# Kernel tuning notes

Measured on AMD Instinct MI355X. Metric: run time of the kernel, lower is better.

Reference implementation:

```python
import jax, jax.numpy as jnp
import numpy as np

B, T, C = 4, 2048, 1024
N_HEAD = 16
HEAD_DIM = C // N_HEAD
SCALE = 1.0 / np.sqrt(HEAD_DIM).astype(np.float32)


def setup_inputs() -> dict:
    key = jax.random.key(0)
    k1, k2, k3 = jax.random.split(key, 3)
    x = jax.random.normal(k1, (B, T, C), dtype=jnp.float32)
    # torch Linear weights: [out_features, in_features], scaled init
    w_qkv = jax.random.normal(k2, (3 * C, C), dtype=jnp.float32) * (1.0 / np.sqrt(C))
    w_out = jax.random.normal(k3, (C, C), dtype=jnp.float32) * (1.0 / np.sqrt(C))
    b_out = jnp.zeros((C,), dtype=jnp.float32)
    return {"x": x, "w_qkv": w_qkv, "w_out": w_out, "b_out": b_out}


def reference(x, w_qkv, w_out, b_out):
    Bsz, Tlen, Cdim = x.shape
    qkv = jnp.einsum('btc,oc->bto', x, w_qkv)  # [B,T,3C]
    q, k, v = jnp.split(qkv, 3, axis=-1)
    # [B,H,T,D]
    def heads(t):
        return t.reshape(Bsz, Tlen, N_HEAD, HEAD_DIM).transpose(0, 2, 1, 3)
    q, k, v = heads(q), heads(k), heads(v)
    att = jnp.einsum('bhqd,bhkd->bhqk', q, k) * SCALE  # [B,H,T,T]
    causal = jnp.tril(jnp.ones((Tlen, Tlen), dtype=bool))
    att = jnp.where(causal[None, None], att, -jnp.inf)
    att = jax.nn.softmax(att, axis=-1)
    out = jnp.einsum('bhqk,bhkd->bhqd', att, v)
    out = out.transpose(0, 2, 1, 3).reshape(Bsz, Tlen, Cdim)
    out = jnp.einsum('btc,oc->bto', out, w_out) + b_out
    return out
```

## Files before the change

### kernel.cpp

```cpp
#include <hip/hip_runtime.h>
#include <stdint.h>


typedef __attribute__((ext_vector_type(8))) short bf16x8;
typedef __attribute__((ext_vector_type(4))) float f32x4;

#define EXP2F(x) __builtin_amdgcn_exp2f(x)
#define SL2E 0.18033688011112042f
#define FIXED_M 15.0f

template <bool B> struct BoolC { static constexpr bool value = B; };

__device__ __forceinline__ short f2bf(float f) {
  union { float f; unsigned u; } c; c.f = f;
  unsigned u = c.u;
  unsigned r = (u + 0x7fffu + ((u >> 16) & 1u)) >> 16;
  return (short)(unsigned short)r;
}

__device__ __forceinline__ void softmax_pack(const f32x4* sc, bf16x8& pa0, bf16x8& pa1) {
  union U { int i[4]; bf16x8 v; };
  U u0, u1;
#pragma unroll
  for (int j = 0; j < 4; ++j) {
    float p0 = EXP2F(sc[j][0]);
    float p1 = EXP2F(sc[j][1]);
    float p2 = EXP2F(sc[j][2]);
    float p3 = EXP2F(sc[j][3]);
    int w0, w1;
    asm("v_cvt_pk_bf16_f32 %0, %1, %2" : "=v"(w0) : "v"(p0), "v"(p1));
    asm("v_cvt_pk_bf16_f32 %0, %1, %2" : "=v"(w1) : "v"(p2), "v"(p3));
    if (j < 2) { u0.i[j * 2] = w0; u0.i[j * 2 + 1] = w1; }
    else       { u1.i[(j - 2) * 2] = w0; u1.i[(j - 2) * 2 + 1] = w1; }
  }
  pa0 = u0.v;
  pa1 = u1.v;
}

__device__ __forceinline__ void llds16(const short* g, short* l) {
  __builtin_amdgcn_global_load_lds(
      (const __attribute__((address_space(1))) unsigned int*)g,
      (__attribute__((address_space(3))) unsigned int*)l, 16, 0, 0);
}

__global__ __launch_bounds__(256) void cast_f32_to_bf16(
    const float* __restrict__ src, short* __restrict__ dst, int n4) {
  int i = blockIdx.x * 256 + threadIdx.x;
  if (i >= n4) return;
  float4 f = ((const float4*)src)[i];
  short4 o;
  o.x = f2bf(f.x); o.y = f2bf(f.y); o.z = f2bf(f.z); o.w = f2bf(f.w);
  ((short4*)dst)[i] = o;
}

__global__ __launch_bounds__(256) void gemm_qkv(
    const short* __restrict__ A, const short* __restrict__ Bw,
    short* __restrict__ Qo, short* __restrict__ Ko, short* __restrict__ Vt) {
  const int K = 1024;
  __shared__ short smem[17408];
  const int tid = threadIdx.x;
  const int lane = tid & 63;
  const int wave = tid >> 6;
  const int m0 = blockIdx.y * 128;
  const int n0 = blockIdx.x * 128;
  const int wm = (wave >> 1) * 64;
  const int wn = (wave & 1) * 64;
  const int mrow = lane & 15;
  const int kq = lane >> 4;

  f32x4 acc[4][4];
#pragma unroll
  for (int i = 0; i < 4; ++i)
#pragma unroll
    for (int j = 0; j < 4; ++j) acc[i][j] = (f32x4){0.f, 0.f, 0.f, 0.f};

  auto stage = [&](int it, int buf) {
#pragma unroll
    for (int call = 0; call < 2; ++call) {
      const int cb = call * 256 + wave * 64;
      const int c = cb + lane;
      const int row = c >> 2;
      const int scol = (c & 3) ^ (row & 3);
      llds16(A + (size_t)(m0 + row) * K + it * 32 + scol * 8,
             &smem[buf * 8192 + cb * 8]);
      llds16(Bw + (size_t)(n0 + row) * K + it * 32 + scol * 8,
             &smem[buf * 8192 + 4096 + cb * 8]);
    }
  };

  stage(0, 0);
  __syncthreads();

  for (int it = 0; it < 32; ++it) {
    const int buf = it & 1;
    if (it < 31) stage(it + 1, buf ^ 1);
    const short* lA = &smem[buf * 8192];
    const short* lB = &smem[buf * 8192 + 4096];
    bf16x8 af[4], bfr[4];
#pragma unroll
    for (int i = 0; i < 4; ++i) {
      const int row = wm + i * 16 + mrow;
      af[i] = *(const bf16x8*)&lA[row * 32 + ((kq ^ (row & 3)) * 8)];
    }
#pragma unroll
    for (int j = 0; j < 4; ++j) {
      const int row = wn + j * 16 + mrow;
      bfr[j] = *(const bf16x8*)&lB[row * 32 + ((kq ^ (row & 3)) * 8)];
    }
#pragma unroll
    for (int i = 0; i < 4; ++i)
#pragma unroll
      for (int j = 0; j < 4; ++j)
        acc[i][j] = __builtin_amdgcn_mfma_f32_16x16x32_bf16(af[i], bfr[j], acc[i][j], 0, 0, 0);
    __syncthreads();
  }

  const int b = m0 >> 11;
  if (n0 < 2048) {
    short* lC = smem;
#pragma unroll
    for (int i = 0; i < 4; ++i) {
      const int row = wm + i * 16 + kq * 4;
#pragma unroll
      for (int j = 0; j < 4; ++j) {
        const int col = wn + j * 16 + mrow;
        const float sc_ = (((n0 + col) >> 10) == 1) ? SL2E : 1.0f;
#pragma unroll
        for (int r = 0; r < 4; ++r)
          lC[(row + r) * 132 + col] = f2bf(acc[i][j][r] * sc_);
      }
    }
    __syncthreads();
#pragma unroll
    for (int call = 0; call < 8; ++call) {
      const int cc = call * 256 + tid;
      const int row = cc >> 4;
      const int t = (m0 + row) & 2047;
      const int o = n0 + (cc & 15) * 8;
      const int c = o & 1023;
      const int h = c >> 6;
      const int d = c & 63;
      short* dst = (o >> 10) == 0 ? Qo : Ko;
      bf16x8 val = *(const bf16x8*)&lC[row * 132 + (cc & 15) * 8];
      *(bf16x8*)(dst + ((size_t)(b * 16 + h) * 2048 + t) * 64 + d) = val;
    }
  } else {
    short* lCt = smem;
#pragma unroll
    for (int i = 0; i < 4; ++i) {
      const int row = wm + i * 16 + kq * 4;
#pragma unroll
      for (int j = 0; j < 4; ++j) {
        const int col = wn + j * 16 + mrow;
#pragma unroll
        for (int r = 0; r < 4; ++r)
          lCt[col * 136 + row + r] = f2bf(acc[i][j][r]);
      }
    }
    __syncthreads();
#pragma unroll
    for (int call = 0; call < 8; ++call) {
      const int cc = call * 256 + tid;
      const int col = cc >> 4;
      const int tg = cc & 15;
      const int o = n0 + col;
      const int d = o & 63;
      const int h = (o >> 6) & 15;
      const int t = (m0 & 2047) + tg * 8;
      bf16x8 val = *(const bf16x8*)&lCt[col * 136 + tg * 8];
      *(bf16x8*)(Vt + ((size_t)(b * 16 + h) * 64 + d) * 2048 + t) = val;
    }
  }
}

__global__ __launch_bounds__(256) void gemm_out(
    const short* __restrict__ A, const short* __restrict__ Bw,
    const float* __restrict__ bias, float* __restrict__ Out) {
  const int K = 1024;
  __shared__ short smem[16384];
  const int tid = threadIdx.x;
  const int lane = tid & 63;
  const int wave = tid >> 6;
  const int m0 = blockIdx.y * 128;
  const int n0 = blockIdx.x * 128;
  const int wm = (wave >> 1) * 64;
  const int wn = (wave & 1) * 64;
  const int mrow = lane & 15;
  const int kq = lane >> 4;

  f32x4 acc[4][4];
#pragma unroll
  for (int i = 0; i < 4; ++i)
#pragma unroll
    for (int j = 0; j < 4; ++j) acc[i][j] = (f32x4){0.f, 0.f, 0.f, 0.f};

  auto stage = [&](int it, int buf) {
#pragma unroll
    for (int call = 0; call < 2; ++call) {
      const int cb = call * 256 + wave * 64;
      const int c = cb + lane;
      const int row = c >> 2;
      const int scol = (c & 3) ^ (row & 3);
      llds16(A + (size_t)(m0 + row) * K + it * 32 + scol * 8,
             &smem[buf * 8192 + cb * 8]);
      llds16(Bw + (size_t)(n0 + row) * K + it * 32 + scol * 8,
             &smem[buf * 8192 + 4096 + cb * 8]);
    }
  };

  stage(0, 0);
  __syncthreads();

  for (int it = 0; it < 32; ++it) {
    const int buf = it & 1;
    if (it < 31) stage(it + 1, buf ^ 1);
    const short* lA = &smem[buf * 8192];
    const short* lB = &smem[buf * 8192 + 4096];
    bf16x8 af[4], bfr[4];
#pragma unroll
    for (int i = 0; i < 4; ++i) {
      const int row = wm + i * 16 + mrow;
      af[i] = *(const bf16x8*)&lA[row * 32 + ((kq ^ (row & 3)) * 8)];
    }
#pragma unroll
    for (int j = 0; j < 4; ++j) {
      const int row = wn + j * 16 + mrow;
      bfr[j] = *(const bf16x8*)&lB[row * 32 + ((kq ^ (row & 3)) * 8)];
    }
#pragma unroll
    for (int i = 0; i < 4; ++i)
#pragma unroll
      for (int j = 0; j < 4; ++j)
        acc[i][j] = __builtin_amdgcn_mfma_f32_16x16x32_bf16(af[i], bfr[j], acc[i][j], 0, 0, 0);
    __syncthreads();
  }

#pragma unroll
  for (int i = 0; i < 4; ++i) {
    const int m = m0 + wm + i * 16 + kq * 4;
#pragma unroll
    for (int j = 0; j < 4; ++j) {
      const int n = n0 + wn + j * 16 + mrow;
      const float bb = bias[n];
#pragma unroll
      for (int r = 0; r < 4; ++r)
        Out[(size_t)(m + r) * 1024 + n] = acc[i][j][r] + bb;
    }
  }
}

__global__ __launch_bounds__(256) void flash_attn(
    const short* __restrict__ Qg, const short* __restrict__ Kg,
    const short* __restrict__ Vtg, short* __restrict__ Og) {
  const int T = 2048;
  __shared__ short lK[2][64 * 64];
  __shared__ short lVt[2][64 * 64];
  const int tid = threadIdx.x;
  const int lane = tid & 63;
  const int wave = tid >> 6;
  const int bh = blockIdx.x;
  const int bx = blockIdx.y;
  const int mrow = lane & 15;
  const int kq = lane >> 4;
  const int swz = mrow & 7;
  const size_t base = (size_t)bh * T * 64;
  const size_t vbase = (size_t)bh * 64 * T;

  const int qt0 = bx;
  const int qt1 = 31 - bx;

  const bf16x8 ones = {0x3F80, 0x3F80, 0x3F80, 0x3F80, 0x3F80, 0x3F80, 0x3F80, 0x3F80};

  bf16x8 aq0_0, aq1_0, aq0_1, aq1_1;
  {
    const short* qp0 = Qg + base + (size_t)(qt0 * 64 + wave * 16 + mrow) * 64 + kq * 8;
    aq0_0 = *(const bf16x8*)qp0;
    aq1_0 = *(const bf16x8*)(qp0 + 32);
    const short* qp1 = Qg + base + (size_t)(qt1 * 64 + wave * 16 + mrow) * 64 + kq * 8;
    aq0_1 = *(const bf16x8*)qp1;
    aq1_1 = *(const bf16x8*)(qp1 + 32);
  }

  f32x4 acc0[4], acc1[4], lac0, lac1;
  lac0 = (f32x4){0.f, 0.f, 0.f, 0.f};
  lac1 = (f32x4){0.f, 0.f, 0.f, 0.f};
#pragma unroll
  for (int jd = 0; jd < 4; ++jd) {
    acc0[jd] = (f32x4){0.f, 0.f, 0.f, 0.f};
    acc1[jd] = (f32x4){0.f, 0.f, 0.f, 0.f};
  }

  auto stage = [&](int nt, int buf) {
#pragma unroll
    for (int call = 0; call < 2; ++call) {
      const int cb = call * 256 + wave * 64;
      const int c = cb + lane;
      const int row = c >> 3;
      const int scol = (c & 7) ^ (row & 7);
      const int grow = (row & 0x23) | ((row & 0x0C) << 1) | ((row & 0x10) >> 2);
      llds16(Kg + base + (size_t)(nt * 64 + grow) * 64 + scol * 8, &lK[buf][cb * 8]);
      llds16(Vtg + vbase + (size_t)row * T + nt * 64 + scol * 8, &lVt[buf][cb * 8]);
    }
  };

  stage(0, 0);
  __syncthreads();

  auto seg = [&](auto A, const short* K_, const short* Vt_, int kt) {
    constexpr bool ACT0 = decltype(A)::value;
    f32x4 sc0[4], sc1[4];
#pragma unroll
    for (int j = 0; j < 4; ++j) {
      const short* krow = &K_[(j * 16 + mrow) * 64];
      bf16x8 kb0 = *(const bf16x8*)&krow[(kq ^ swz) * 8];
      bf16x8 kb1 = *(const bf16x8*)&krow[((4 + kq) ^ swz) * 8];
      __builtin_amdgcn_s_setprio(1);
      f32x4 ss = (f32x4){-FIXED_M, -FIXED_M, -FIXED_M, -FIXED_M};
      ss = __builtin_amdgcn_mfma_f32_16x16x32_bf16(kb0, aq0_1, ss, 0, 0, 0);
      ss = __builtin_amdgcn_mfma_f32_16x16x32_bf16(kb1, aq1_1, ss, 0, 0, 0);
      sc1[j] = ss;
      if constexpr (ACT0) {
        f32x4 s2 = (f32x4){-FIXED_M, -FIXED_M, -FIXED_M, -FIXED_M};
        s2 = __builtin_amdgcn_mfma_f32_16x16x32_bf16(kb0, aq0_0, s2, 0, 0, 0);
        s2 = __builtin_amdgcn_mfma_f32_16x16x32_bf16(kb1, aq1_0, s2, 0, 0, 0);
        sc0[j] = s2;
      }
      __builtin_amdgcn_s_setprio(0);
    }

    if (kt == qt1) {
      const int qcol = qt1 * 64 + wave * 16 + mrow;
#pragma unroll
      for (int j = 0; j < 4; ++j) {
        const int keyb = kt * 64 + ((j & 2) << 4) + (kq << 3) + ((j & 1) << 2);
#pragma unroll
        for (int r = 0; r < 4; ++r)
          if (keyb + r > qcol) sc1[j][r] = -1e30f;
      }
    }
    if constexpr (ACT0) {
      if (kt == qt0) {
        const int qcol = qt0 * 64 + wave * 16 + mrow;
#pragma unroll
        for (int j = 0; j < 4; ++j) {
          const int keyb = kt * 64 + ((j & 2) << 4) + (kq << 3) + ((j & 1) << 2);
#pragma unroll
          for (int r = 0; r < 4; ++r)
            if (keyb + r > qcol) sc0[j][r] = -1e30f;
        }
      }
    }

    bf16x8 pa0_1, pa1_1, pa0_0, pa1_0;
    softmax_pack(sc1, pa0_1, pa1_1);
    lac1 = __builtin_amdgcn_mfma_f32_16x16x32_bf16(pa0_1, ones, lac1, 0, 0, 0);
    lac1 = __builtin_amdgcn_mfma_f32_16x16x32_bf16(pa1_1, ones, lac1, 0, 0, 0);
    if constexpr (ACT0) {
      softmax_pack(sc0, pa0_0, pa1_0);
      lac0 = __builtin_amdgcn_mfma_f32_16x16x32_bf16(pa0_0, ones, lac0, 0, 0, 0);
      lac0 = __builtin_amdgcn_mfma_f32_16x16x32_bf16(pa1_0, ones, lac0, 0, 0, 0);
    }

#pragma unroll
    for (int jd = 0; jd < 4; ++jd) {
      const short* vrow = &Vt_[(jd * 16 + mrow) * 64];
      bf16x8 vb0 = *(const bf16x8*)&vrow[(kq ^ swz) * 8];
      bf16x8 vb1 = *(const bf16x8*)&vrow[((4 + kq) ^ swz) * 8];
      __builtin_amdgcn_s_setprio(1);
      acc1[jd] = __builtin_amdgcn_mfma_f32_16x16x32_bf16(pa0_1, vb0, acc1[jd], 0, 0, 0);
      acc1[jd] = __builtin_amdgcn_mfma_f32_16x16x32_bf16(pa1_1, vb1, acc1[jd], 0, 0, 0);
      if constexpr (ACT0) {
        acc0[jd] = __builtin_amdgcn_mfma_f32_16x16x32_bf16(pa0_0, vb0, acc0[jd], 0, 0, 0);
        acc0[jd] = __builtin_amdgcn_mfma_f32_16x16x32_bf16(pa1_0, vb1, acc0[jd], 0, 0, 0);
      }
      __builtin_amdgcn_s_setprio(0);
    }
  };

  for (int kt = 0; kt <= qt1; ++kt) {
    const int bcur = kt & 1;
    if (kt < qt1) stage(kt + 1, bcur ^ 1);
    if (kt <= qt0) seg(BoolC<true>{}, lK[bcur], lVt[bcur], kt);
    else           seg(BoolC<false>{}, lK[bcur], lVt[bcur], kt);
    __syncthreads();
  }

  const int b = bh >> 4;
  const int h = bh & 15;
#pragma unroll
  for (int r = 0; r < 4; ++r) {
    const float inv0 = 1.0f / lac0[r];
    const int t0 = qt0 * 64 + wave * 16 + kq * 4 + r;
#pragma unroll
    for (int jd = 0; jd < 4; ++jd) {
      const int col = h * 64 + jd * 16 + mrow;
      Og[((size_t)b * 2048 + t0) * 1024 + col] = f2bf(acc0[jd][r] * inv0);
    }
    const float inv1 = 1.0f / lac1[r];
    const int t1 = qt1 * 64 + wave * 16 + kq * 4 + r;
#pragma unroll
    for (int jd = 0; jd < 4; ++jd) {
      const int col = h * 64 + jd * 16 + mrow;
      Og[((size_t)b * 2048 + t1) * 1024 + col] = f2bf(acc1[jd][r] * inv1);
    }
  }
}

extern "C" void kernel_launch(void* const* d_in, const int* in_sizes, int n_in,
                              void* d_out, int out_size, void* d_ws, size_t ws_size,
                              hipStream_t stream) {
  const float* x = (const float*)d_in[0];
  const float* w_qkv = (const float*)d_in[1];
  const float* w_out = (const float*)d_in[2];
  const float* b_out = (const float*)d_in[3];
  float* out = (float*)d_out;

  char* ws = (char*)d_ws;
  const size_t NX = 8192ull * 1024;
  const size_t NWQ = 3072ull * 1024;
  const size_t NWO = 1024ull * 1024;
  const size_t NQ = 64ull * 2048 * 64;
  size_t off = 0;
  short* xb    = (short*)(ws + off); off += NX * 2;
  short* wqkvb = (short*)(ws + off); off += NWQ * 2;
  short* woutb = (short*)(ws + off); off += NWO * 2;
  short* q     = (short*)(ws + off); off += NQ * 2;
  short* k     = (short*)(ws + off); off += NQ * 2;
  short* vt    = (short*)(ws + off); off += NQ * 2;
  short* attb  = (short*)(ws + off); off += NX * 2;
  if (off > ws_size) return;

  cast_f32_to_bf16<<<(int)(NX / 4 / 256), 256, 0, stream>>>(x, xb, (int)(NX / 4));
  cast_f32_to_bf16<<<(int)(NWQ / 4 / 256), 256, 0, stream>>>(w_qkv, wqkvb, (int)(NWQ / 4));
  cast_f32_to_bf16<<<(int)(NWO / 4 / 256), 256, 0, stream>>>(w_out, woutb, (int)(NWO / 4));
  gemm_qkv<<<dim3(24, 64), 256, 0, stream>>>(xb, wqkvb, q, k, vt);
  flash_attn<<<dim3(64, 16), 256, 0, stream>>>(q, k, vt, attb);
  gemm_out<<<dim3(8, 64), 256, 0, stream>>>(attb, woutb, b_out, out);
}
```

Measured before the change: 255.1 us.

## Enlarge QKV GEMM tiles to 256x256 with a 4-stage LDS prefetch pipeline

The QKV projection GEMM moves from 128x128 tiles with 256 threads to 256x256 tiles with 512 threads. It also replaces double buffering with a four-slot LDS ring driven by explicit vmcnt waits, raw barriers and MFMA priority hints. The goal is more operand reuse per global load and better hiding of load latency. The epilogue becomes two passes through LDS because the larger tile does not fit at once. The block now uses 128KB of LDS, which limits each CU to one block, and the 384-block grid may leave the last wave partly idle.

```diff
diff --git a/kernel.cpp b/kernel.cpp
--- a/kernel.cpp
+++ b/kernel.cpp
@@ -53,122 +53,147 @@
   ((short4*)dst)[i] = o;
 }
 
-__global__ __launch_bounds__(256) void gemm_qkv(
+__global__ __launch_bounds__(512, 2) void gemm_qkv(
     const short* __restrict__ A, const short* __restrict__ Bw,
     short* __restrict__ Qo, short* __restrict__ Ko, short* __restrict__ Vt) {
   const int K = 1024;
-  __shared__ short smem[17408];
+  __shared__ short smem[65536];
   const int tid = threadIdx.x;
   const int lane = tid & 63;
   const int wave = tid >> 6;
-  const int m0 = blockIdx.y * 128;
-  const int n0 = blockIdx.x * 128;
-  const int wm = (wave >> 1) * 64;
-  const int wn = (wave & 1) * 64;
+  const int wr = wave >> 2;
+  const int wc = wave & 3;
+  const int m0 = blockIdx.y * 256;
+  const int n0 = blockIdx.x * 256;
   const int mrow = lane & 15;
   const int kq = lane >> 4;
 
-  f32x4 acc[4][4];
-#pragma unroll
-  for (int i = 0; i < 4; ++i)
+  f32x4 acc[8][4];
+#pragma unroll
+  for (int i = 0; i < 8; ++i)
 #pragma unroll
     for (int j = 0; j < 4; ++j) acc[i][j] = (f32x4){0.f, 0.f, 0.f, 0.f};
 
-  auto stage = [&](int it, int buf) {
+  auto stage = [&](int it, int slot) {
+    short* sb = &smem[slot * 16384];
 #pragma unroll
     for (int call = 0; call < 2; ++call) {
-      const int cb = call * 256 + wave * 64;
+      const int cb = call * 512 + wave * 64;
       const int c = cb + lane;
       const int row = c >> 2;
-      const int scol = (c & 3) ^ (row & 3);
-      llds16(A + (size_t)(m0 + row) * K + it * 32 + scol * 8,
-             &smem[buf * 8192 + cb * 8]);
-      llds16(Bw + (size_t)(n0 + row) * K + it * 32 + scol * 8,
-             &smem[buf * 8192 + 4096 + cb * 8]);
+      const int scol = (c & 3) ^ ((row ^ (row >> 2)) & 3);
+      llds16(A + (size_t)(m0 + row) * K + it * 32 + scol * 8, &sb[cb * 8]);
+      llds16(Bw + (size_t)(n0 + row) * K + it * 32 + scol * 8, &sb[8192 + cb * 8]);
     }
   };
 
-  stage(0, 0);
-  __syncthreads();
-
-  for (int it = 0; it < 32; ++it) {
-    const int buf = it & 1;
-    if (it < 31) stage(it + 1, buf ^ 1);
-    const short* lA = &smem[buf * 8192];
-    const short* lB = &smem[buf * 8192 + 4096];
-    bf16x8 af[4], bfr[4];
-#pragma unroll
-    for (int i = 0; i < 4; ++i) {
-      const int row = wm + i * 16 + mrow;
-      af[i] = *(const bf16x8*)&lA[row * 32 + ((kq ^ (row & 3)) * 8)];
+  auto body = [&](int kt) {
+    __builtin_amdgcn_s_barrier();
+    __builtin_amdgcn_sched_barrier(0);
+    const short* lA = &smem[(kt & 3) * 16384];
+    const short* lB = lA + 8192;
+    bf16x8 af[8], bfr[4];
+#pragma unroll
+    for (int i = 0; i < 8; ++i) {
+      const int row = wr * 128 + i * 16 + mrow;
+      af[i] = *(const bf16x8*)&lA[row * 32 + (((kq ^ row ^ (row >> 2)) & 3) * 8)];
     }
 #pragma unroll
     for (int j = 0; j < 4; ++j) {
-      const int row = wn + j * 16 + mrow;
-      bfr[j] = *(const bf16x8*)&lB[row * 32 + ((kq ^ (row & 3)) * 8)];
-    }
-#pragma unroll
-    for (int i = 0; i < 4; ++i)
+      const int row = wc * 64 + j * 16 + mrow;
+      bfr[j] = *(const bf16x8*)&lB[row * 32 + (((kq ^ row ^ (row >> 2)) & 3) * 8)];
+    }
+    __builtin_amdgcn_s_setprio(1);
+#pragma unroll
+    for (int i = 0; i < 8; ++i)
 #pragma unroll
       for (int j = 0; j < 4; ++j)
         acc[i][j] = __builtin_amdgcn_mfma_f32_16x16x32_bf16(af[i], bfr[j], acc[i][j], 0, 0, 0);
-    __syncthreads();
-  }
+    __builtin_amdgcn_s_setprio(0);
+    __builtin_amdgcn_sched_barrier(0);
+    __builtin_amdgcn_s_barrier();
+  };
+
+  stage(0, 0); stage(1, 1); stage(2, 2);
+  for (int kt = 0; kt < 29; ++kt) {
+    stage(kt + 3, (kt + 3) & 3);
+    asm volatile("s_waitcnt vmcnt(12)" ::: "memory");
+    body(kt);
+  }
+  asm volatile("s_waitcnt vmcnt(8)" ::: "memory");
+  body(29);
+  asm volatile("s_waitcnt vmcnt(4)" ::: "memory");
+  body(30);
+  asm volatile("s_waitcnt vmcnt(0)" ::: "memory");
+  body(31);
 
   const int b = m0 >> 11;
   if (n0 < 2048) {
+    const float sc_ = ((n0 >> 10) == 1) ? SL2E : 1.0f;
     short* lC = smem;
-#pragma unroll
-    for (int i = 0; i < 4; ++i) {
-      const int row = wm + i * 16 + kq * 4;
-#pragma unroll
-      for (int j = 0; j < 4; ++j) {
-        const int col = wn + j * 16 + mrow;
-        const float sc_ = (((n0 + col) >> 10) == 1) ? SL2E : 1.0f;
-#pragma unroll
-        for (int r = 0; r < 4; ++r)
-          lC[(row + r) * 132 + col] = f2bf(acc[i][j][r] * sc_);
-      }
-    }
-    __syncthreads();
-#pragma unroll
-    for (int call = 0; call < 8; ++call) {
-      const int cc = call * 256 + tid;
-      const int row = cc >> 4;
-      const int t = (m0 + row) & 2047;
-      const int o = n0 + (cc & 15) * 8;
-      const int c = o & 1023;
-      const int h = c >> 6;
-      const int d = c & 63;
-      short* dst = (o >> 10) == 0 ? Qo : Ko;
-      bf16x8 val = *(const bf16x8*)&lC[row * 132 + (cc & 15) * 8];
-      *(bf16x8*)(dst + ((size_t)(b * 16 + h) * 2048 + t) * 64 + d) = val;
+#pragma unroll 1
+    for (int p = 0; p < 2; ++p) {
+      if (p) __syncthreads();
+      if (wr == p) {
+#pragma unroll
+        for (int i = 0; i < 8; ++i) {
+          const int rl = i * 16 + kq * 4;
+#pragma unroll
+          for (int j = 0; j < 4; ++j) {
+            const int col = wc * 64 + j * 16 + mrow;
+#pragma unroll
+            for (int r = 0; r < 4; ++r)
+              lC[(rl + r) * 260 + col] = f2bf(acc[i][j][r] * sc_);
+          }
+        }
+      }
+      __syncthreads();
+#pragma unroll
+      for (int call = 0; call < 8; ++call) {
+        const int cc = call * 512 + tid;
+        const int row = cc >> 5;
+        const int ch = cc & 31;
+        const int t = (m0 + p * 128 + row) & 2047;
+        const int o = n0 + ch * 8;
+        const int c = o & 1023;
+        const int h = c >> 6;
+        const int d = c & 63;
+        short* dst = (o >> 10) == 0 ? Qo : Ko;
+        bf16x8 val = *(const bf16x8*)&lC[row * 260 + ch * 8];
+        *(bf16x8*)(dst + ((size_t)(b * 16 + h) * 2048 + t) * 64 + d) = val;
+      }
     }
   } else {
     short* lCt = smem;
-#pragma unroll
-    for (int i = 0; i < 4; ++i) {
-      const int row = wm + i * 16 + kq * 4;
-#pragma unroll
-      for (int j = 0; j < 4; ++j) {
-        const int col = wn + j * 16 + mrow;
-#pragma unroll
-        for (int r = 0; r < 4; ++r)
-          lCt[col * 136 + row + r] = f2bf(acc[i][j][r]);
-      }
-    }
-    __syncthreads();
-#pragma unroll
-    for (int call = 0; call < 8; ++call) {
-      const int cc = call * 256 + tid;
-      const int col = cc >> 4;
-      const int tg = cc & 15;
-      const int o = n0 + col;
-      const int d = o & 63;
-      const int h = (o >> 6) & 15;
-      const int t = (m0 & 2047) + tg * 8;
-      bf16x8 val = *(const bf16x8*)&lCt[col * 136 + tg * 8];
-      *(bf16x8*)(Vt + ((size_t)(b * 16 + h) * 64 + d) * 2048 + t) = val;
+#pragma unroll 1
+    for (int p = 0; p < 2; ++p) {
+      if (p) __syncthreads();
+      if (wr == p) {
+#pragma unroll
+        for (int i = 0; i < 8; ++i) {
+          const int rl = i * 16 + kq * 4;
+#pragma unroll
+          for (int j = 0; j < 4; ++j) {
+            const int col = wc * 64 + j * 16 + mrow;
+#pragma unroll
+            for (int r = 0; r < 4; ++r)
+              lCt[col * 136 + rl + r] = f2bf(acc[i][j][r]);
+          }
+        }
+      }
+      __syncthreads();
+#pragma unroll
+      for (int call = 0; call < 8; ++call) {
+        const int cc = call * 512 + tid;
+        const int col = cc >> 4;
+        const int tg = cc & 15;
+        const int o = n0 + col;
+        const int d = o & 63;
+        const int h = (o >> 6) & 15;
+        const int t = (m0 & 2047) + p * 128 + tg * 8;
+        bf16x8 val = *(const bf16x8*)&lCt[col * 136 + tg * 8];
+        *(bf16x8*)(Vt + ((size_t)(b * 16 + h) * 64 + d) * 2048 + t) = val;
+      }
     }
   }
 }
@@ -306,8 +331,8 @@
   stage(0, 0);
   __syncthreads();
 
-  auto seg = [&](auto A, const short* K_, const short* Vt_, int kt) {
-    constexpr bool ACT0 = decltype(A)::value;
+  auto seg = [&](auto Aa, const short* K_, const short* Vt_, int kt) {
+    constexpr bool ACT0 = decltype(Aa)::value;
     f32x4 sc0[4], sc1[4];
 #pragma unroll
     for (int j = 0; j < 4; ++j) {
@@ -433,7 +458,7 @@
   cast_f32_to_bf16<<<(int)(NX / 4 / 256), 256, 0, stream>>>(x, xb, (int)(NX / 4));
   cast_f32_to_bf16<<<(int)(NWQ / 4 / 256), 256, 0, stream>>>(w_qkv, wqkvb, (int)(NWQ / 4));
   cast_f32_to_bf16<<<(int)(NWO / 4 / 256), 256, 0, stream>>>(w_out, woutb, (int)(NWO / 4));
-  gemm_qkv<<<dim3(24, 64), 256, 0, stream>>>(xb, wqkvb, q, k, vt);
+  gemm_qkv<<<dim3(12, 32), 512, 0, stream>>>(xb, wqkvb, q, k, vt);
   flash_attn<<<dim3(64, 16), 256, 0, stream>>>(q, k, vt, attb);
   gemm_out<<<dim3(8, 64), 256, 0, stream>>>(attb, woutb, b_out, out);
 }
```

Result: slower. 262.8 us (+3.0%).
